# Kernel optimization log

Hardware: AMD Instinct MI355X
Metric: run time of the kernel (lower is better)

## Reference

```python
import jax, jax.numpy as jnp
import numpy as np

TAU = 2.0   # membrane decay time constant
TH = 1.0    # firing threshold

N, T, D = 64, 64, 8192


def setup_inputs() -> dict:
    key = jax.random.key(0)
    k1, k2, k3 = jax.random.split(key, 3)
    x = jax.random.normal(k1, (N, T, D), dtype=jnp.float32)
    momentum = jax.random.uniform(k2, (1,), dtype=jnp.float32)
    lamb = jax.random.uniform(k3, (1,), dtype=jnp.float32)
    return {"x": x, "momentum": momentum, "lamb": lamb}


def reference(x, momentum, lamb):
    """Momentum LIF neuron scanned over the time axis.

    Assumed dynamics (CUDA kernel source unavailable; reduces to standard
    STBP hard-reset LIF when momentum == 0 and lamb == 0):
        v_t = momentum * v_{t-1} + x_t - lamb * u_{t-1}   # momentum on input current
        u_t = (1 - 1/tau) * u_{t-1} + v_t                 # leaky integrate
        s_t = H(u_t - th)                                 # spike
        u_t = u_t * (1 - s_t)                             # hard reset
    x: [N, T, D] -> spikes: [N, T, D]
    """
    decay = 1.0 - 1.0 / TAU
    mom = momentum[0]
    lb = lamb[0]

    def step(carry, xt):
        u, v = carry                      # each [N, D]
        v = mom * v + xt - lb * u
        u = decay * u + v
        s = (u >= TH).astype(xt.dtype)
        u = u * (1.0 - s)                 # hard reset
        return (u, v), s

    xs = jnp.swapaxes(x, 0, 1)            # [T, N, D] for time scan
    u0 = jnp.zeros_like(x[:, 0])
    v0 = jnp.zeros_like(x[:, 0])
    _, spikes = jax.lax.scan(step, (u0, v0), xs)
    return jnp.swapaxes(spikes, 0, 1)      # [N, T, D]
```

## Files before the change

kernel.cpp:

```cpp
#include <hip/hip_runtime.h>
#include <stdint.h>


#define N_ 64
#define T_ 64
#define D_ 8192
#define PF 16

typedef __attribute__((ext_vector_type(4))) float f32x4;

__global__ __launch_bounds__(256) void lif_compute_pack(
    const float* __restrict__ x,
    const float* __restrict__ momp,
    const float* __restrict__ lambp,
    uint2* __restrict__ ws)
{
#pragma clang fp contract(off)
    float mom  = momp[0];
    float lamb = lambp[0];
    const float decay = 0.5f;

    asm volatile("" : "+s"(mom), "+s"(lamb));

    const int tid = blockIdx.x * blockDim.x + threadIdx.x;
    const int n = tid >> 13;
    const int d = tid & (D_ - 1);
    const float* xp = x + (size_t)n * T_ * D_ + d;

    asm volatile("s_waitcnt vmcnt(0)" ::: "memory");

    float xs[PF];
#pragma unroll
    for (int i = 0; i < PF; ++i) {
        const float* a = xp + (size_t)i * D_;
        asm volatile("global_load_dword %0, %1, off" : "=v"(xs[i]) : "v"(a));
    }

    float u = 0.f, v = 0.f;
    uint32_t blo = 0u, bhi = 0u;

#pragma unroll
    for (int t = 0; t < T_ - PF; ++t) {
        const int slot = t & (PF - 1);
        asm volatile("s_waitcnt vmcnt(15)" : "+v"(xs[slot]));
        const float xt = xs[slot];
        const float* a = xp + (size_t)(t + PF) * D_;
        asm volatile("global_load_dword %0, %1, off" : "=v"(xs[slot]) : "v"(a));

        float t1 = mom * v;
        float t2 = lamb * u;
        v = (t1 + xt) - t2;
        u = decay * u + v;
        const bool sp = (u >= 1.0f);
        if (t < 32) blo |= ((uint32_t)sp) << t;
        else        bhi |= ((uint32_t)sp) << (t - 32);
        u = sp ? 0.0f : u;
    }

    asm volatile("s_waitcnt vmcnt(0)"
                 : "+v"(xs[0]),  "+v"(xs[1]),  "+v"(xs[2]),  "+v"(xs[3]),
                   "+v"(xs[4]),  "+v"(xs[5]),  "+v"(xs[6]),  "+v"(xs[7]),
                   "+v"(xs[8]),  "+v"(xs[9]),  "+v"(xs[10]), "+v"(xs[11]),
                   "+v"(xs[12]), "+v"(xs[13]), "+v"(xs[14]), "+v"(xs[15]));

#pragma unroll
    for (int t = T_ - PF; t < T_; ++t) {
        const float xt = xs[t & (PF - 1)];
        float t1 = mom * v;
        float t2 = lamb * u;
        v = (t1 + xt) - t2;
        u = decay * u + v;
        const bool sp = (u >= 1.0f);
        if (t < 32) blo |= ((uint32_t)sp) << t;
        else        bhi |= ((uint32_t)sp) << (t - 32);
        u = sp ? 0.0f : u;
    }

    ws[tid] = make_uint2(blo, bhi);
}

__global__ __launch_bounds__(256) void lif_expand(
    const uint2* __restrict__ ws,
    float* __restrict__ out)
{
    const int g = blockIdx.x * blockDim.x + threadIdx.x;
    const size_t e = (size_t)g << 2;
    const int nt = (int)(e >> 13);
    const int t  = nt & (T_ - 1);
    const int n  = nt >> 6;
    const int d  = (int)(e & (D_ - 1));
    const int chain = (n << 13) + d;

    const uint2 w0 = ws[chain + 0];
    const uint2 w1 = ws[chain + 1];
    const uint2 w2 = ws[chain + 2];
    const uint2 w3 = ws[chain + 3];

    const int  sh = t & 31;
    const bool hi = (t >= 32);

    f32x4 o;
    o.x = (((hi ? w0.y : w0.x) >> sh) & 1u) ? 1.0f : 0.0f;
    o.y = (((hi ? w1.y : w1.x) >> sh) & 1u) ? 1.0f : 0.0f;
    o.z = (((hi ? w2.y : w2.x) >> sh) & 1u) ? 1.0f : 0.0f;
    o.w = (((hi ? w3.y : w3.x) >> sh) & 1u) ? 1.0f : 0.0f;

    __builtin_nontemporal_store(o, reinterpret_cast<f32x4*>(out) + g);
}

extern "C" void kernel_launch(void* const* d_in, const int* in_sizes, int n_in,
                              void* d_out, int out_size, void* d_ws, size_t ws_size,
                              hipStream_t stream) {
    const float* x    = (const float*)d_in[0];
    const float* momp = (const float*)d_in[1];
    const float* lamb = (const float*)d_in[2];
    float* out = (float*)d_out;
    uint2* ws  = (uint2*)d_ws;

    {
        dim3 block(256);
        dim3 grid((N_ * D_) / 256);
        hipLaunchKernelGGL(lif_compute_pack, grid, block, 0, stream,
                           x, momp, lamb, ws);
    }
    {
        dim3 block(256);
        dim3 grid((N_ * T_ * D_ / 4) / 256);
        hipLaunchKernelGGL(lif_expand, grid, block, 0, stream, ws, out);
    }
}
```

Before: 231.7 us.

## Fuse LIF scan and spike expansion into one vectorized kernel

Replaces the two-kernel pipeline (scan packing spikes into bitmasks, then a separate expand kernel) with one kernel that writes float spikes directly with nontemporal vector stores. Each thread now handles four adjacent channels using 16-byte loads, and the prefetch depth drops from 16 to 8 vectors. This removes the workspace round trip and one launch, but cuts thread count by four, which lowers parallelism for latency hiding on a purely bandwidth-bound stream. It also drops the hand-written asm waitcnt pipelining in favour of compiler-scheduled loads.

Measured after the change: 244.7 us. +5.6%, slower.

```diff
diff --git a/kernel.cpp b/kernel.cpp
--- a/kernel.cpp
+++ b/kernel.cpp
@@ -5,107 +5,74 @@
 #define N_ 64
 #define T_ 64
 #define D_ 8192
-#define PF 16
+#define PF 8
+#define CPT 4
 
 typedef __attribute__((ext_vector_type(4))) float f32x4;
 
-__global__ __launch_bounds__(256) void lif_compute_pack(
+__global__ __launch_bounds__(256) void lif_fused(
     const float* __restrict__ x,
     const float* __restrict__ momp,
     const float* __restrict__ lambp,
-    uint2* __restrict__ ws)
+    float* __restrict__ out)
 {
 #pragma clang fp contract(off)
-    float mom  = momp[0];
-    float lamb = lambp[0];
+    const float mom   = momp[0];
+    const float lamb  = lambp[0];
     const float decay = 0.5f;
 
-    asm volatile("" : "+s"(mom), "+s"(lamb));
+    const int g  = blockIdx.x * blockDim.x + threadIdx.x;
+    const int n  = g >> 11;
+    const int dq = g & 2047;
+    const size_t base = (size_t)n * (size_t)(T_ * D_) + ((size_t)dq << 2);
 
-    const int tid = blockIdx.x * blockDim.x + threadIdx.x;
-    const int n = tid >> 13;
-    const int d = tid & (D_ - 1);
-    const float* xp = x + (size_t)n * T_ * D_ + d;
+    const f32x4* __restrict__ xv = reinterpret_cast<const f32x4*>(x + base);
+    f32x4* __restrict__ ov       = reinterpret_cast<f32x4*>(out + base);
+    const int RS = D_ / 4;
 
-    asm volatile("s_waitcnt vmcnt(0)" ::: "memory");
+    f32x4 buf[PF];
+#pragma unroll
+    for (int i = 0; i < PF; ++i) buf[i] = xv[(size_t)i * RS];
 
-    float xs[PF];
-#pragma unroll
-    for (int i = 0; i < PF; ++i) {
-        const float* a = xp + (size_t)i * D_;
-        asm volatile("global_load_dword %0, %1, off" : "=v"(xs[i]) : "v"(a));
-    }
-
-    float u = 0.f, v = 0.f;
-    uint32_t blo = 0u, bhi = 0u;
+    float u[CPT] = {0.f, 0.f, 0.f, 0.f};
+    float v[CPT] = {0.f, 0.f, 0.f, 0.f};
 
 #pragma unroll
     for (int t = 0; t < T_ - PF; ++t) {
-        const int slot = t & (PF - 1);
-        asm volatile("s_waitcnt vmcnt(15)" : "+v"(xs[slot]));
-        const float xt = xs[slot];
-        const float* a = xp + (size_t)(t + PF) * D_;
-        asm volatile("global_load_dword %0, %1, off" : "=v"(xs[slot]) : "v"(a));
+        const f32x4 xt = buf[t & (PF - 1)];
+        buf[t & (PF - 1)] = xv[(size_t)(t + PF) * RS];
 
-        float t1 = mom * v;
-        float t2 = lamb * u;
-        v = (t1 + xt) - t2;
-        u = decay * u + v;
-        const bool sp = (u >= 1.0f);
-        if (t < 32) blo |= ((uint32_t)sp) << t;
-        else        bhi |= ((uint32_t)sp) << (t - 32);
-        u = sp ? 0.0f : u;
+        f32x4 o;
+#pragma unroll
+        for (int c = 0; c < CPT; ++c) {
+            const float t1 = mom * v[c];
+            const float t2 = lamb * u[c];
+            v[c] = (t1 + xt[c]) - t2;
+            u[c] = decay * u[c] + v[c];
+            const bool sp = (u[c] >= 1.0f);
+            o[c] = sp ? 1.0f : 0.0f;
+            u[c] = sp ? 0.0f : u[c];
+        }
+        __builtin_nontemporal_store(o, ov + (size_t)t * RS);
     }
-
-    asm volatile("s_waitcnt vmcnt(0)"
-                 : "+v"(xs[0]),  "+v"(xs[1]),  "+v"(xs[2]),  "+v"(xs[3]),
-                   "+v"(xs[4]),  "+v"(xs[5]),  "+v"(xs[6]),  "+v"(xs[7]),
-                   "+v"(xs[8]),  "+v"(xs[9]),  "+v"(xs[10]), "+v"(xs[11]),
-                   "+v"(xs[12]), "+v"(xs[13]), "+v"(xs[14]), "+v"(xs[15]));
 
 #pragma unroll
     for (int t = T_ - PF; t < T_; ++t) {
-        const float xt = xs[t & (PF - 1)];
-        float t1 = mom * v;
-        float t2 = lamb * u;
-        v = (t1 + xt) - t2;
-        u = decay * u + v;
-        const bool sp = (u >= 1.0f);
-        if (t < 32) blo |= ((uint32_t)sp) << t;
-        else        bhi |= ((uint32_t)sp) << (t - 32);
-        u = sp ? 0.0f : u;
+        const f32x4 xt = buf[t & (PF - 1)];
+
+        f32x4 o;
+#pragma unroll
+        for (int c = 0; c < CPT; ++c) {
+            const float t1 = mom * v[c];
+            const float t2 = lamb * u[c];
+            v[c] = (t1 + xt[c]) - t2;
+            u[c] = decay * u[c] + v[c];
+            const bool sp = (u[c] >= 1.0f);
+            o[c] = sp ? 1.0f : 0.0f;
+            u[c] = sp ? 0.0f : u[c];
+        }
+        __builtin_nontemporal_store(o, ov + (size_t)t * RS);
     }
-
-    ws[tid] = make_uint2(blo, bhi);
-}
-
-__global__ __launch_bounds__(256) void lif_expand(
-    const uint2* __restrict__ ws,
-    float* __restrict__ out)
-{
-    const int g = blockIdx.x * blockDim.x + threadIdx.x;
-    const size_t e = (size_t)g << 2;
-    const int nt = (int)(e >> 13);
-    const int t  = nt & (T_ - 1);
-    const int n  = nt >> 6;
-    const int d  = (int)(e & (D_ - 1));
-    const int chain = (n << 13) + d;
-
-    const uint2 w0 = ws[chain + 0];
-    const uint2 w1 = ws[chain + 1];
-    const uint2 w2 = ws[chain + 2];
-    const uint2 w3 = ws[chain + 3];
-
-    const int  sh = t & 31;
-    const bool hi = (t >= 32);
-
-    f32x4 o;
-    o.x = (((hi ? w0.y : w0.x) >> sh) & 1u) ? 1.0f : 0.0f;
-    o.y = (((hi ? w1.y : w1.x) >> sh) & 1u) ? 1.0f : 0.0f;
-    o.z = (((hi ? w2.y : w2.x) >> sh) & 1u) ? 1.0f : 0.0f;
-    o.w = (((hi ? w3.y : w3.x) >> sh) & 1u) ? 1.0f : 0.0f;
-
-    __builtin_nontemporal_store(o, reinterpret_cast<f32x4*>(out) + g);
 }
 
 extern "C" void kernel_launch(void* const* d_in, const int* in_sizes, int n_in,
@@ -115,17 +82,8 @@
     const float* momp = (const float*)d_in[1];
     const float* lamb = (const float*)d_in[2];
     float* out = (float*)d_out;
-    uint2* ws  = (uint2*)d_ws;
 
-    {
-        dim3 block(256);
-        dim3 grid((N_ * D_) / 256);
-        hipLaunchKernelGGL(lif_compute_pack, grid, block, 0, stream,
-                           x, momp, lamb, ws);
-    }
-    {
-        dim3 block(256);
-        dim3 grid((N_ * T_ * D_ / 4) / 256);
-        hipLaunchKernelGGL(lif_expand, grid, block, 0, stream, ws, out);
-    }
+    dim3 block(256);
+    dim3 grid((N_ * D_ / CPT) / 256);
+    hipLaunchKernelGGL(lif_fused, grid, block, 0, stream, x, momp, lamb, out);
 }
```
